# Performance work log

Measured on AMD Instinct MI355X. Metric: run time of the kernel, lower is better.

Reference implementation:

```python
import jax, jax.numpy as jnp
import numpy as np

EPS = 1e-6
NH, DK, DV = 4, 32, 32

def _ln2d(x, w, b):
    # LayerNorm2d: normalize over channel dim (dim=1), biased variance
    mu = jnp.mean(x, axis=1, keepdims=True)
    var = jnp.mean((x - mu) ** 2, axis=1, keepdims=True)
    y = (x - mu) / jnp.sqrt(var + EPS)
    return w[None, :, None, None] * y + b[None, :, None, None]

def _c1x1(w, x):
    # 1x1 conv == per-pixel matmul: w [out,in], x [B,C,H,W]
    return jnp.einsum('oc,bchw->bohw', w, x)

def _shifts(x, r):
    # All (2r+1)^2 zero-padded spatial shifts, row-major (dy,dx) like nn.Unfold.
    B, C, H, W = x.shape
    xp = jnp.pad(x, ((0, 0), (0, 0), (r, r), (r, r)))
    return jnp.stack([xp[:, :, dy:dy + H, dx:dx + W]
                      for dy in range(2 * r + 1) for dx in range(2 * r + 1)], axis=0)

def _local_attn(q, k, v, kernel):
    # Correlation-pyramid local attention: per-pixel q.k over kxk window of k,
    # softmax over window (temperature sqrt(d_k)), weighted sum of v window
    # (weights shared across channels, per ChannelAttention).
    B, _, H, W = q.shape
    r = (kernel - 1) // 2
    K2 = kernel * kernel
    qh = q.reshape(B, NH, DK, H, W)
    ks = _shifts(k, r).reshape(K2, B, NH, DK, H, W)
    corr = jnp.einsum('bncyx,jbncyx->jbnyx', qh, ks)            # [K2,B,NH,H,W]
    attn = jax.nn.softmax(corr / jnp.sqrt(jnp.float32(DK)), axis=0)
    vs = _shifts(v, r).reshape(K2, B, NH, DV, H, W)
    out = jnp.einsum('jbnyx,jbncyx->bncyx', attn, vs)
    return out.reshape(B, NH * DV, H, W)

def _mha(q, k, v, kernel, wq, wk, wv, fc, lnw, lnb):
    resid = q
    heads = _local_attn(_c1x1(wq, q), _c1x1(wk, k), _c1x1(wv, v), kernel)
    out = _c1x1(fc, heads) + resid   # residual BEFORE LN (per source)
    return _ln2d(out, lnw, lnb)

def _ffn(x, w1, b1, w2, b2, lnw, lnb):
    h = jax.nn.relu(_c1x1(w1, x) + b1[None, :, None, None])
    y = _c1x1(w2, h) + b2[None, :, None, None]
    return _ln2d(y, lnw, lnb) + x    # LN BEFORE residual add (per source)

def setup_inputs():
    key = jax.random.key(0)
    ks = jax.random.split(key, 24)
    B, C, H, W = 4, 128, 96, 96
    s = (2.0 / C) ** 0.5
    f = jnp.float32
    return {
        'input1': jax.random.normal(ks[0], (B, C, H, W), f),
        'input2': jax.random.normal(ks[1], (B, C, H, W), f),
        'wq_s': jax.random.normal(ks[2], (NH * DK, C), f) * s,
        'wk_s': jax.random.normal(ks[3], (NH * DK, C), f) * s,
        'wv_s': jax.random.normal(ks[4], (NH * DV, C), f) * s,
        'fc_s': jax.random.normal(ks[5], (C, NH * DV), f) * s,
        'lnw_s': jnp.ones((C,), f),
        'lnb_s': jnp.zeros((C,), f),
        'wq_c': jax.random.normal(ks[6], (NH * DK, C), f) * s,
        'wk_c': jax.random.normal(ks[7], (NH * DK, C), f) * s,
        'wv_c': jax.random.normal(ks[8], (NH * DV, C), f) * s,
        'fc_c': jax.random.normal(ks[9], (C, NH * DV), f) * s,
        'lnw_c': jnp.ones((C,), f),
        'lnb_c': jnp.zeros((C,), f),
        'w1': jax.random.normal(ks[10], (C, C), f) * s,
        'b1': jnp.zeros((C,), f),
        'w2': jax.random.normal(ks[11], (C, C), f) * s,
        'b2': jnp.zeros((C,), f),
        'lnw_f': jnp.ones((C,), f),
        'lnb_f': jnp.zeros((C,), f),
        'kernel': 5,
        'pad': 2,
    }

def reference(input1, input2, wq_s, wk_s, wv_s, fc_s, lnw_s, lnb_s,
              wq_c, wk_c, wv_c, fc_c, lnw_c, lnb_c,
              w1, b1, w2, b2, lnw_f, lnb_f, kernel, pad):
    slf1 = _mha(input1, input1, input1, kernel, wq_s, wk_s, wv_s, fc_s, lnw_s, lnb_s)
    slf2 = _mha(input2, input2, input2, kernel, wq_s, wk_s, wv_s, fc_s, lnw_s, lnb_s)
    crs1 = _mha(slf1, slf2, slf2, kernel, wq_c, wk_c, wv_c, fc_c, lnw_c, lnb_c)
    crs2 = _mha(slf2, slf1, slf1, kernel, wq_c, wk_c, wv_c, fc_c, lnw_c, lnb_c)
    out1 = _ffn(crs1, w1, b1, w2, b2, lnw_f, lnb_f)
    out2 = _ffn(crs2, w1, b1, w2, b2, lnw_f, lnb_f)
    return (out1, out2)
```

## Files before the change

kernel.cpp:

```cpp
#include <hip/hip_runtime.h>
#include <hip/hip_bf16.h>

typedef _Float16 h16;
typedef __attribute__((ext_vector_type(8))) _Float16 f16x8v;
typedef __attribute__((ext_vector_type(2))) _Float16 h2v;
typedef __attribute__((ext_vector_type(4))) float f32x4;
#define DI __device__ __forceinline__

constexpr int CH = 128;
constexpr int HH = 96, WW = 96;
constexpr int HW = HH * WW;
constexpr int NB = 4;
constexpr int NPIX = NB * HW;
constexpr int LDT = 136;
constexpr size_t HP = (size_t)NPIX * 32;
constexpr int GH = NPIX / 64;
constexpr int TY = 4, TX = 32;
constexpr int HYH = TY + 4, HXH = TX + 4;
constexpr int LDC = 40;
constexpr int ATB = NPIX / (TY * TX) * 4;

struct __attribute__((aligned(16))) h16x8 { h16 h[8]; };
struct Set { h16 *q, *k, *v; };

DI float h2f(h16 x) { return (float)x; }
DI h16   f2h(float x) { return (h16)x; }


DI void stage_x_cl(const h16* __restrict__ src, int ldx, h16* xl, int t) {
    #pragma unroll
    for (int i = 0; i < 4; ++i) {
        int id = t + 256 * i, px = id >> 4, cc = (id & 15) * 8;
        *reinterpret_cast<f16x8v*>(&xl[px * LDT + cc]) =
            *reinterpret_cast<const f16x8v*>(&src[(size_t)px * ldx + cc]);
    }
}

DI void stage_x_pl(const float* __restrict__ src, h16* xl, int t) {
    #pragma unroll
    for (int i = 0; i < 8; ++i) {
        int id = t + 256 * i, c = id >> 4, p4 = (id & 15) * 4;
        float4 v = *reinterpret_cast<const float4*>(&src[(size_t)c * HW + p4]);
        xl[(p4 + 0) * LDT + c] = f2h(v.x);
        xl[(p4 + 1) * LDT + c] = f2h(v.y);
        xl[(p4 + 2) * LDT + c] = f2h(v.z);
        xl[(p4 + 3) * LDT + c] = f2h(v.w);
    }
}

DI void stage_x_hm(const h16* __restrict__ Tq, h16* xl, int p0, int t) {
    const int px = t >> 2, c8 = (t & 3) * 8;
    #pragma unroll
    for (int h = 0; h < 4; ++h)
        *reinterpret_cast<f16x8v*>(&xl[px * LDT + h * 32 + c8]) =
            *reinterpret_cast<const f16x8v*>(&Tq[(size_t)h * HP + (size_t)(p0 + px) * 32 + c8]);
}

DI void stage_w(const float* __restrict__ w, h16* wl, int t) {
    #pragma unroll
    for (int i = 0; i < 8; ++i) {
        int id = t + 256 * i, o = id >> 4, cc = (id & 15) * 8;
        float4 a = *reinterpret_cast<const float4*>(&w[o * CH + cc]);
        float4 b = *reinterpret_cast<const float4*>(&w[o * CH + cc + 4]);
        h16x8 tmp;
        tmp.h[0] = f2h(a.x); tmp.h[1] = f2h(a.y); tmp.h[2] = f2h(a.z); tmp.h[3] = f2h(a.w);
        tmp.h[4] = f2h(b.x); tmp.h[5] = f2h(b.y); tmp.h[6] = f2h(b.z); tmp.h[7] = f2h(b.w);
        *reinterpret_cast<f16x8v*>(&wl[o * LDT + cc]) = *reinterpret_cast<const f16x8v*>(&tmp);
    }
}

DI void gemm64(const h16* xl, const h16* wl, int w, int l, f32x4* acc) {
    const int s = l & 15, g = l >> 4;
    #pragma unroll
    for (int ks = 0; ks < 4; ++ks) {
        f16x8v a = *reinterpret_cast<const f16x8v*>(&xl[(16 * w + s) * LDT + ks * 32 + g * 8]);
        #pragma unroll
        for (int n = 0; n < 8; ++n) {
            f16x8v b = *reinterpret_cast<const f16x8v*>(&wl[(16 * n + s) * LDT + ks * 32 + g * 8]);
            acc[n] = __builtin_amdgcn_mfma_f32_16x16x32_f16(a, b, acc[n], 0, 0, 0);
        }
    }
}

DI void qkv_epi(const f32x4* acc, h16* comp, int p0, int w, int l) {
    const int s = l & 15, g = l >> 4;
    #pragma unroll
    for (int n = 0; n < 8; ++n) {
        const int o = 16 * n + s, head = o >> 5, ch = o & 31;
        h16* pl = comp + (size_t)head * HP;
        #pragma unroll
        for (int j = 0; j < 4; ++j) {
            int px = 16 * w + 4 * g + j;
            pl[(size_t)(p0 + px) * 32 + ch] = f2h(acc[n][j]);
        }
    }
}

DI void ln128(float r[8][4], const float* gm, const float* bt, float val[8][4]) {
    #pragma unroll
    for (int j = 0; j < 4; ++j) {
        float sm = 0.f, sq = 0.f;
        #pragma unroll
        for (int n = 0; n < 8; ++n) { float v = r[n][j]; sm += v; sq += v * v; }
        sm += __shfl_xor(sm, 1); sq += __shfl_xor(sq, 1);
        sm += __shfl_xor(sm, 2); sq += __shfl_xor(sq, 2);
        sm += __shfl_xor(sm, 4); sq += __shfl_xor(sq, 4);
        sm += __shfl_xor(sm, 8); sq += __shfl_xor(sq, 8);
        const float mu = sm * (1.f / 128.f);
        const float var = sq * (1.f / 128.f) - mu * mu;
        const float rs = rsqrtf(var + 1e-6f);
        #pragma unroll
        for (int n = 0; n < 8; ++n)
            val[n][j] = gm[n] * (r[n][j] - mu) * rs + bt[n];
    }
}

__global__ __launch_bounds__(256, 2)
void qkv_self_b(const float* __restrict__ x0, const float* __restrict__ x1,
                const float* __restrict__ w0, const float* __restrict__ w1_,
                const float* __restrict__ w2_, Set sA, Set sB) {
    __shared__ h16 xl[64 * LDT];
    __shared__ h16 wl[CH * LDT];
    const int bid = blockIdx.x, half = bid / GH, p0 = (bid % GH) * 64;
    const float* xv = half ? x1 : x0;
    Set S = half ? sB : sA;
    const int t = threadIdx.x;
    const int b = p0 / HW, hw0 = p0 % HW;
    stage_x_pl(xv + (size_t)b * CH * HW + hw0, xl, t);
    const int w = t >> 6, l = t & 63;
    #pragma unroll
    for (int m = 0; m < 3; ++m) {
        const float* wm = (m == 0) ? w0 : ((m == 1) ? w1_ : w2_);
        h16* comp = (m == 0) ? S.q : ((m == 1) ? S.k : S.v);
        __syncthreads();
        stage_w(wm, wl, t);
        __syncthreads();
        f32x4 acc[8];
        #pragma unroll
        for (int n = 0; n < 8; ++n) acc[n] = {0.f, 0.f, 0.f, 0.f};
        gemm64(xl, wl, w, l, acc);
        qkv_epi(acc, comp, p0, w, l);
    }
}

__global__ __launch_bounds__(256)
void attn5b(Set s0, Set s1) {
    __shared__ h16 kv[HYH * HXH * LDC];
    const int bid = blockIdx.x, setId = bid / ATB, id = bid - setId * ATB;
    Set S = setId ? s1 : s0;
    const int n = id & 3, tile = id >> 2;
    const int img = tile / 72, rem = tile % 72, tr = rem / 3, tc = rem % 3;
    const int y0 = tr * TY, x0 = tc * TX;
    const int t = threadIdx.x;
    const int p = t >> 1, half = t & 1, ch16 = half * 16;
    const int ty = p >> 5, tx = p & 31;
    h16* Qh = S.q + (size_t)n * HP;
    const h16* Kh = S.k + (size_t)n * HP;
    const h16* Vh = S.v + (size_t)n * HP;
    const int gp = img * HW + (y0 + ty) * WW + (x0 + tx);
    h16* qp = Qh + (size_t)gp * 32 + ch16;

    f16x8v q0 = *reinterpret_cast<const f16x8v*>(qp);
    f16x8v q1 = *reinterpret_cast<const f16x8v*>(qp + 8);
    {
        const h16 sc = (h16)0.17677669529663689f;
        #pragma unroll
        for (int e = 0; e < 8; ++e) { q0[e] *= sc; q1[e] *= sc; }
    }

    #pragma unroll
    for (int i = 0; i < 5; ++i) {
        int id2 = t + 256 * i;
        if (id2 < 1152) {
            int r = id2 / 144, c = id2 - r * 144, px = c >> 2, c8 = (c & 3) * 8;
            int y = y0 + r - 2, x = x0 + px - 2;
            f16x8v v = {0, 0, 0, 0, 0, 0, 0, 0};
            if ((unsigned)y < (unsigned)HH && (unsigned)x < (unsigned)WW)
                v = *reinterpret_cast<const f16x8v*>(&Kh[((size_t)(img * HW + y * WW + x)) * 32 + c8]);
            *reinterpret_cast<f16x8v*>(&kv[(r * HXH + px) * LDC + c8]) = v;
        }
    }
    __syncthreads();

    float corr[25];
    #pragma unroll
    for (int dy = 0; dy < 5; ++dy)
        #pragma unroll
        for (int dx = 0; dx < 5; ++dx) {
            const h16* kp = &kv[((ty + dy) * HXH + tx + dx) * LDC + ch16];
            f16x8v k0 = *reinterpret_cast<const f16x8v*>(kp);
            f16x8v k1 = *reinterpret_cast<const f16x8v*>(kp + 8);
            float s;
#if __has_builtin(__builtin_amdgcn_fdot2)
            s = __builtin_amdgcn_fdot2(h2v{q0[0], q0[1]}, h2v{k0[0], k0[1]}, 0.f, false);
            s = __builtin_amdgcn_fdot2(h2v{q0[2], q0[3]}, h2v{k0[2], k0[3]}, s, false);
            s = __builtin_amdgcn_fdot2(h2v{q0[4], q0[5]}, h2v{k0[4], k0[5]}, s, false);
            s = __builtin_amdgcn_fdot2(h2v{q0[6], q0[7]}, h2v{k0[6], k0[7]}, s, false);
            s = __builtin_amdgcn_fdot2(h2v{q1[0], q1[1]}, h2v{k1[0], k1[1]}, s, false);
            s = __builtin_amdgcn_fdot2(h2v{q1[2], q1[3]}, h2v{k1[2], k1[3]}, s, false);
            s = __builtin_amdgcn_fdot2(h2v{q1[4], q1[5]}, h2v{k1[4], k1[5]}, s, false);
            s = __builtin_amdgcn_fdot2(h2v{q1[6], q1[7]}, h2v{k1[6], k1[7]}, s, false);
#else
            s = 0.f;
            #pragma unroll
            for (int e = 0; e < 8; ++e) s += h2f(q0[e]) * h2f(k0[e]);
            #pragma unroll
            for (int e = 0; e < 8; ++e) s += h2f(q1[e]) * h2f(k1[e]);
#endif
            s += __shfl_xor(s, 1);
            corr[dy * 5 + dx] = s;
        }

    float m = corr[0];
    #pragma unroll
    for (int j = 1; j < 25; ++j) m = fmaxf(m, corr[j]);
    float sum = 0.f;
    #pragma unroll
    for (int j = 0; j < 25; ++j) {
        float e = __expf(corr[j] - m);
        corr[j] = e; sum += e;
    }
    const float inv = 1.f / sum;

    __syncthreads();
    #pragma unroll
    for (int i = 0; i < 5; ++i) {
        int id2 = t + 256 * i;
        if (id2 < 1152) {
            int r = id2 / 144, c = id2 - r * 144, px = c >> 2, c8 = (c & 3) * 8;
            int y = y0 + r - 2, x = x0 + px - 2;
            f16x8v v = {0, 0, 0, 0, 0, 0, 0, 0};
            if ((unsigned)y < (unsigned)HH && (unsigned)x < (unsigned)WW)
                v = *reinterpret_cast<const f16x8v*>(&Vh[((size_t)(img * HW + y * WW + x)) * 32 + c8]);
            *reinterpret_cast<f16x8v*>(&kv[(r * HXH + px) * LDC + c8]) = v;
        }
    }
    __syncthreads();

    f16x8v o0 = {0, 0, 0, 0, 0, 0, 0, 0};
    f16x8v o1 = {0, 0, 0, 0, 0, 0, 0, 0};
    #pragma unroll
    for (int dy = 0; dy < 5; ++dy)
        #pragma unroll
        for (int dx = 0; dx < 5; ++dx) {
            const h16 ah = f2h(corr[dy * 5 + dx]);
            const f16x8v av = {ah, ah, ah, ah, ah, ah, ah, ah};
            const h16* vp = &kv[((ty + dy) * HXH + tx + dx) * LDC + ch16];
            f16x8v v0 = *reinterpret_cast<const f16x8v*>(vp);
            f16x8v v1 = *reinterpret_cast<const f16x8v*>(vp + 8);
            o0 += av * v0;
            o1 += av * v1;
        }
    {
        const h16 ih = f2h(inv);
        const f16x8v iv = {ih, ih, ih, ih, ih, ih, ih, ih};
        o0 *= iv; o1 *= iv;
    }
    *reinterpret_cast<f16x8v*>(qp)     = o0;
    *reinterpret_cast<f16x8v*>(qp + 8) = o1;
}

__global__ __launch_bounds__(256, 2)
void fcx_b(const h16* __restrict__ tA, const h16* __restrict__ tB,
           const float* __restrict__ in1, const float* __restrict__ in2,
           const float* __restrict__ wfc, const float* __restrict__ gamma,
           const float* __restrict__ beta,
           const float* __restrict__ wq, const float* __restrict__ wk,
           const float* __restrict__ wv,
           h16* __restrict__ x1g, h16* __restrict__ x2g, Set c1, Set c2) {
    __shared__ h16 xA[64 * LDT];
    __shared__ h16 xB[64 * LDT];
    __shared__ h16 wl[CH * LDT];
    const int t = threadIdx.x, p0 = blockIdx.x * 64;
    const int w = t >> 6, l = t & 63, s = l & 15, g4 = l >> 4;
    const int b = p0 / HW, hw0 = p0 % HW;

    stage_x_hm(tA, xA, p0, t);
    stage_x_hm(tB, xB, p0, t);
    stage_w(wfc, wl, t);
    __syncthreads();

    float gm[8], bt[8];
    #pragma unroll
    for (int n = 0; n < 8; ++n) { gm[n] = gamma[16 * n + s]; bt[n] = beta[16 * n + s]; }

    h16 vA[8][4], vB[8][4];
    {
        f32x4 acc[8];
        #pragma unroll
        for (int n = 0; n < 8; ++n) acc[n] = {0.f, 0.f, 0.f, 0.f};
        gemm64(xA, wl, w, l, acc);
        float r[8][4], val[8][4];
        #pragma unroll
        for (int n = 0; n < 8; ++n) {
            const int o = 16 * n + s;
            #pragma unroll
            for (int j = 0; j < 4; ++j) {
                const int px = 16 * w + 4 * g4 + j;
                r[n][j] = acc[n][j] +
                    in1[(size_t)b * CH * HW + (size_t)o * HW + hw0 + px];
            }
        }
        ln128(r, gm, bt, val);
        #pragma unroll
        for (int n = 0; n < 8; ++n)
            #pragma unroll
            for (int j = 0; j < 4; ++j) vA[n][j] = f2h(val[n][j]);
    }
    {
        f32x4 acc[8];
        #pragma unroll
        for (int n = 0; n < 8; ++n) acc[n] = {0.f, 0.f, 0.f, 0.f};
        gemm64(xB, wl, w, l, acc);
        float r[8][4], val[8][4];
        #pragma unroll
        for (int n = 0; n < 8; ++n) {
            const int o = 16 * n + s;
            #pragma unroll
            for (int j = 0; j < 4; ++j) {
                const int px = 16 * w + 4 * g4 + j;
                r[n][j] = acc[n][j] +
                    in2[(size_t)b * CH * HW + (size_t)o * HW + hw0 + px];
            }
        }
        ln128(r, gm, bt, val);
        #pragma unroll
        for (int n = 0; n < 8; ++n)
            #pragma unroll
            for (int j = 0; j < 4; ++j) vB[n][j] = f2h(val[n][j]);
    }
    __syncthreads();
    #pragma unroll
    for (int n = 0; n < 8; ++n) {
        const int o = 16 * n + s;
        #pragma unroll
        for (int j = 0; j < 4; ++j) {
            const int px = 16 * w + 4 * g4 + j;
            xA[px * LDT + o] = vA[n][j];
            xB[px * LDT + o] = vB[n][j];
            x1g[(size_t)(p0 + px) * CH + o] = vA[n][j];
            x2g[(size_t)(p0 + px) * CH + o] = vB[n][j];
        }
    }
    __syncthreads();

    stage_w(wq, wl, t);
    __syncthreads();
    {
        f32x4 acc[8];
        #pragma unroll
        for (int n = 0; n < 8; ++n) acc[n] = {0.f, 0.f, 0.f, 0.f};
        gemm64(xA, wl, w, l, acc);
        qkv_epi(acc, c1.q, p0, w, l);
    }
    {
        f32x4 acc[8];
        #pragma unroll
        for (int n = 0; n < 8; ++n) acc[n] = {0.f, 0.f, 0.f, 0.f};
        gemm64(xB, wl, w, l, acc);
        qkv_epi(acc, c2.q, p0, w, l);
    }
    __syncthreads();
    stage_w(wk, wl, t);
    __syncthreads();
    {
        f32x4 acc[8];
        #pragma unroll
        for (int n = 0; n < 8; ++n) acc[n] = {0.f, 0.f, 0.f, 0.f};
        gemm64(xB, wl, w, l, acc);
        qkv_epi(acc, c1.k, p0, w, l);
    }
    {
        f32x4 acc[8];
        #pragma unroll
        for (int n = 0; n < 8; ++n) acc[n] = {0.f, 0.f, 0.f, 0.f};
        gemm64(xA, wl, w, l, acc);
        qkv_epi(acc, c2.k, p0, w, l);
    }
    __syncthreads();
    stage_w(wv, wl, t);
    __syncthreads();
    {
        f32x4 acc[8];
        #pragma unroll
        for (int n = 0; n < 8; ++n) acc[n] = {0.f, 0.f, 0.f, 0.f};
        gemm64(xB, wl, w, l, acc);
        qkv_epi(acc, c1.v, p0, w, l);
    }
    {
        f32x4 acc[8];
        #pragma unroll
        for (int n = 0; n < 8; ++n) acc[n] = {0.f, 0.f, 0.f, 0.f};
        gemm64(xA, wl, w, l, acc);
        qkv_epi(acc, c2.v, p0, w, l);
    }
}

__global__ __launch_bounds__(256, 2)
void ffn_ln_b(const h16* __restrict__ t0, const h16* __restrict__ t1,
              const h16* __restrict__ x0, const h16* __restrict__ x1,
              const float* __restrict__ wfc, const float* __restrict__ gc,
              const float* __restrict__ bc,
              const float* __restrict__ w1m, const float* __restrict__ b1v,
              const float* __restrict__ w2m, const float* __restrict__ b2v,
              const float* __restrict__ gf, const float* __restrict__ bf,
              float* __restrict__ o0, float* __restrict__ o1) {
    __shared__ __align__(16) char smem[64 * LDT * 2 * 2 + CH * LDT * 2];
    h16*   xl = (h16*)smem;
    h16*   yl = (h16*)(smem + 64 * LDT * 2);
    h16*   wl = (h16*)(smem + 64 * LDT * 2 * 2);
    float* ll = (float*)(smem + 64 * LDT * 2 * 2);
    const int bid = blockIdx.x, half = bid / GH, p0 = (bid % GH) * 64;
    const h16* tin = half ? t1 : t0;
    const h16* xg  = half ? x1 : x0;
    float* outp = half ? o1 : o0;
    const int t = threadIdx.x;
    const int w = t >> 6, l = t & 63, s = l & 15, g4 = l >> 4;

    stage_x_hm(tin, xl, p0, t);
    stage_w(wfc, wl, t);
    __syncthreads();

    h16 yv[8][4];
    {
        f32x4 acc[8];
        #pragma unroll
        for (int n = 0; n < 8; ++n) acc[n] = {0.f, 0.f, 0.f, 0.f};
        gemm64(xl, wl, w, l, acc);
        float gm[8], bt[8], r[8][4], val[8][4];
        #pragma unroll
        for (int n = 0; n < 8; ++n) { gm[n] = gc[16 * n + s]; bt[n] = bc[16 * n + s]; }
        #pragma unroll
        for (int n = 0; n < 8; ++n) {
            const int o = 16 * n + s;
            #pragma unroll
            for (int j = 0; j < 4; ++j) {
                const int px = 16 * w + 4 * g4 + j;
                r[n][j] = acc[n][j] + h2f(xg[(size_t)(p0 + px) * CH + o]);
            }
        }
        ln128(r, gm, bt, val);
        #pragma unroll
        for (int n = 0; n < 8; ++n)
            #pragma unroll
            for (int j = 0; j < 4; ++j) yv[n][j] = f2h(val[n][j]);
    }
    __syncthreads();
    #pragma unroll
    for (int n = 0; n < 8; ++n) {
        const int o = 16 * n + s;
        #pragma unroll
        for (int j = 0; j < 4; ++j)
            yl[(16 * w + 4 * g4 + j) * LDT + o] = yv[n][j];
    }
    stage_w(w1m, wl, t);
    __syncthreads();

    {
        f32x4 acc[8];
        #pragma unroll
        for (int n = 0; n < 8; ++n) acc[n] = {0.f, 0.f, 0.f, 0.f};
        gemm64(yl, wl, w, l, acc);
        #pragma unroll
        for (int n = 0; n < 8; ++n) {
            const int o = 16 * n + s;
            const float bv = b1v[o];
            #pragma unroll
            for (int j = 0; j < 4; ++j)
                xl[(16 * w + 4 * g4 + j) * LDT + o] = f2h(fmaxf(acc[n][j] + bv, 0.f));
        }
    }
    __syncthreads();
    stage_w(w2m, wl, t);
    __syncthreads();

    float val[8][4];
    {
        f32x4 acc[8];
        #pragma unroll
        for (int n = 0; n < 8; ++n) acc[n] = {0.f, 0.f, 0.f, 0.f};
        gemm64(xl, wl, w, l, acc);
        float gm[8], bt[8], r[8][4];
        #pragma unroll
        for (int n = 0; n < 8; ++n) { gm[n] = gf[16 * n + s]; bt[n] = bf[16 * n + s]; }
        #pragma unroll
        for (int n = 0; n < 8; ++n) {
            const int o = 16 * n + s;
            const float bv = b2v[o];
            #pragma unroll
            for (int j = 0; j < 4; ++j) r[n][j] = acc[n][j] + bv;
        }
        ln128(r, gm, bt, val);
        #pragma unroll
        for (int n = 0; n < 8; ++n) {
            const int o = 16 * n + s;
            #pragma unroll
            for (int j = 0; j < 4; ++j)
                val[n][j] += h2f(yl[(16 * w + 4 * g4 + j) * LDT + o]);
        }
    }
    __syncthreads();
    #pragma unroll
    for (int n = 0; n < 8; ++n) {
        const int o = 16 * n + s;
        #pragma unroll
        for (int j = 0; j < 4; ++j) ll[o * 65 + 16 * w + 4 * g4 + j] = val[n][j];
    }
    __syncthreads();
    const int b = p0 / HW, hw0 = p0 % HW;
    #pragma unroll
    for (int i = 0; i < 8; ++i) {
        int id = t + 256 * i, c = id >> 4, p4 = (id & 15) * 4;
        float4 v = { ll[c * 65 + p4], ll[c * 65 + p4 + 1],
                     ll[c * 65 + p4 + 2], ll[c * 65 + p4 + 3] };
        *reinterpret_cast<float4*>(&outp[(size_t)b * CH * HW + (size_t)c * HW + hw0 + p4]) = v;
    }
}

extern "C" void kernel_launch(void* const* d_in, const int* in_sizes, int n_in,
                              void* d_out, int out_size, void* d_ws, size_t ws_size,
                              hipStream_t stream) {
    (void)in_sizes; (void)n_in; (void)out_size; (void)ws_size;
    const float* in1  = (const float*)d_in[0];
    const float* in2  = (const float*)d_in[1];
    const float* wq_s = (const float*)d_in[2];
    const float* wk_s = (const float*)d_in[3];
    const float* wv_s = (const float*)d_in[4];
    const float* fc_s = (const float*)d_in[5];
    const float* lnw_s= (const float*)d_in[6];
    const float* lnb_s= (const float*)d_in[7];
    const float* wq_c = (const float*)d_in[8];
    const float* wk_c = (const float*)d_in[9];
    const float* wv_c = (const float*)d_in[10];
    const float* fc_c = (const float*)d_in[11];
    const float* lnw_c= (const float*)d_in[12];
    const float* lnb_c= (const float*)d_in[13];
    const float* w1   = (const float*)d_in[14];
    const float* b1   = (const float*)d_in[15];
    const float* w2   = (const float*)d_in[16];
    const float* b2   = (const float*)d_in[17];
    const float* lnw_f= (const float*)d_in[18];
    const float* lnb_f= (const float*)d_in[19];

    const size_t BUF  = (size_t)NPIX * CH;
    const size_t BUFB = BUF * 2;
    char* ws = (char*)d_ws;
    h16* W0 = (h16*)(ws + 0 * BUFB);
    h16* W1 = (h16*)(ws + 1 * BUFB);
    h16* W2 = (h16*)(ws + 2 * BUFB);
    h16* W3 = (h16*)(ws + 3 * BUFB);
    h16* D0 = (h16*)d_out;
    h16* D1 = (h16*)((char*)d_out + 1 * BUFB);
    h16* D2 = (h16*)((char*)d_out + 2 * BUFB);
    h16* D3 = (h16*)((char*)d_out + 3 * BUFB);
    float* out1 = (float*)d_out;
    float* out2 = (float*)d_out + BUF;

    const dim3 B(256);

    Set SA = {W0, D0, D1};
    Set SB = {W1, D2, D3};
    h16* X1 = W2;
    h16* X2 = W3;
    Set C1 = {W0, D0, D1};
    Set C2 = {W1, D2, D3};

    qkv_self_b<<<dim3(2 * GH), B, 0, stream>>>(in1, in2, wq_s, wk_s, wv_s, SA, SB);
    attn5b<<<dim3(2 * ATB), B, 0, stream>>>(SA, SB);
    fcx_b<<<dim3(GH), B, 0, stream>>>(SA.q, SB.q, in1, in2,
                                      fc_s, lnw_s, lnb_s,
                                      wq_c, wk_c, wv_c, X1, X2, C1, C2);
    attn5b<<<dim3(2 * ATB), B, 0, stream>>>(C1, C2);
    ffn_ln_b<<<dim3(2 * GH), B, 0, stream>>>(C1.q, C2.q, X1, X2,
                                             fc_c, lnw_c, lnb_c,
                                             w1, b1, w2, b2, lnw_f, lnb_f,
                                             out1, out2);
}
```

Measured before the change: 156.9 us.

## Split fused FC/QKV kernel so each block handles one stream

Each block of the FC+LayerNorm+cross-QKV kernel now processes only one of the two input streams, chosen by block index, and the grid is doubled. This halves the per-block shared-memory footprint (one activation tile instead of two) and doubles the block count, to improve occupancy and load balance across CUs. The cost is that every block now stages the fc, wq, wk and wv weight tiles for half as much GEMM work. One redundant barrier before the first weight restage is also dropped.

```diff
diff --git a/kernel.cpp b/kernel.cpp
--- a/kernel.cpp
+++ b/kernel.cpp
@@ -261,36 +261,38 @@
 }
 
 __global__ __launch_bounds__(256, 2)
-void fcx_b(const h16* __restrict__ tA, const h16* __restrict__ tB,
-           const float* __restrict__ in1, const float* __restrict__ in2,
-           const float* __restrict__ wfc, const float* __restrict__ gamma,
-           const float* __restrict__ beta,
-           const float* __restrict__ wq, const float* __restrict__ wk,
-           const float* __restrict__ wv,
-           h16* __restrict__ x1g, h16* __restrict__ x2g, Set c1, Set c2) {
-    __shared__ h16 xA[64 * LDT];
-    __shared__ h16 xB[64 * LDT];
+void fcx1_b(const h16* __restrict__ tA, const h16* __restrict__ tB,
+            const float* __restrict__ in1, const float* __restrict__ in2,
+            const float* __restrict__ wfc, const float* __restrict__ gamma,
+            const float* __restrict__ beta,
+            const float* __restrict__ wq, const float* __restrict__ wk,
+            const float* __restrict__ wv,
+            h16* __restrict__ x1g, h16* __restrict__ x2g, Set c1, Set c2) {
+    __shared__ h16 xl[64 * LDT];
     __shared__ h16 wl[CH * LDT];
-    const int t = threadIdx.x, p0 = blockIdx.x * 64;
+    const int bid = blockIdx.x, half = bid / GH, p0 = (bid % GH) * 64;
+    const h16*   tin = half ? tB : tA;
+    const float* inr = half ? in2 : in1;
+    h16*         xg  = half ? x2g : x1g;
+    Set own   = half ? c2 : c1;
+    Set other = half ? c1 : c2;
+    const int t = threadIdx.x;
     const int w = t >> 6, l = t & 63, s = l & 15, g4 = l >> 4;
     const int b = p0 / HW, hw0 = p0 % HW;
 
-    stage_x_hm(tA, xA, p0, t);
-    stage_x_hm(tB, xB, p0, t);
+    stage_x_hm(tin, xl, p0, t);
     stage_w(wfc, wl, t);
     __syncthreads();
 
-    float gm[8], bt[8];
-    #pragma unroll
-    for (int n = 0; n < 8; ++n) { gm[n] = gamma[16 * n + s]; bt[n] = beta[16 * n + s]; }
-
-    h16 vA[8][4], vB[8][4];
-    {
-        f32x4 acc[8];
-        #pragma unroll
-        for (int n = 0; n < 8; ++n) acc[n] = {0.f, 0.f, 0.f, 0.f};
-        gemm64(xA, wl, w, l, acc);
-        float r[8][4], val[8][4];
+    h16 vX[8][4];
+    {
+        f32x4 acc[8];
+        #pragma unroll
+        for (int n = 0; n < 8; ++n) acc[n] = {0.f, 0.f, 0.f, 0.f};
+        gemm64(xl, wl, w, l, acc);
+        float gm[8], bt[8], r[8][4], val[8][4];
+        #pragma unroll
+        for (int n = 0; n < 8; ++n) { gm[n] = gamma[16 * n + s]; bt[n] = beta[16 * n + s]; }
         #pragma unroll
         for (int n = 0; n < 8; ++n) {
             const int o = 16 * n + s;
@@ -298,36 +300,14 @@
             for (int j = 0; j < 4; ++j) {
                 const int px = 16 * w + 4 * g4 + j;
                 r[n][j] = acc[n][j] +
-                    in1[(size_t)b * CH * HW + (size_t)o * HW + hw0 + px];
+                    inr[(size_t)b * CH * HW + (size_t)o * HW + hw0 + px];
             }
         }
         ln128(r, gm, bt, val);
         #pragma unroll
         for (int n = 0; n < 8; ++n)
             #pragma unroll
-            for (int j = 0; j < 4; ++j) vA[n][j] = f2h(val[n][j]);
-    }
-    {
-        f32x4 acc[8];
-        #pragma unroll
-        for (int n = 0; n < 8; ++n) acc[n] = {0.f, 0.f, 0.f, 0.f};
-        gemm64(xB, wl, w, l, acc);
-        float r[8][4], val[8][4];
-        #pragma unroll
-        for (int n = 0; n < 8; ++n) {
-            const int o = 16 * n + s;
-            #pragma unroll
-            for (int j = 0; j < 4; ++j) {
-                const int px = 16 * w + 4 * g4 + j;
-                r[n][j] = acc[n][j] +
-                    in2[(size_t)b * CH * HW + (size_t)o * HW + hw0 + px];
-            }
-        }
-        ln128(r, gm, bt, val);
-        #pragma unroll
-        for (int n = 0; n < 8; ++n)
-            #pragma unroll
-            for (int j = 0; j < 4; ++j) vB[n][j] = f2h(val[n][j]);
+            for (int j = 0; j < 4; ++j) vX[n][j] = f2h(val[n][j]);
     }
     __syncthreads();
     #pragma unroll
@@ -336,29 +316,18 @@
         #pragma unroll
         for (int j = 0; j < 4; ++j) {
             const int px = 16 * w + 4 * g4 + j;
-            xA[px * LDT + o] = vA[n][j];
-            xB[px * LDT + o] = vB[n][j];
-            x1g[(size_t)(p0 + px) * CH + o] = vA[n][j];
-            x2g[(size_t)(p0 + px) * CH + o] = vB[n][j];
-        }
-    }
-    __syncthreads();
-
+            xl[px * LDT + o] = vX[n][j];
+            xg[(size_t)(p0 + px) * CH + o] = vX[n][j];
+        }
+    }
     stage_w(wq, wl, t);
     __syncthreads();
     {
         f32x4 acc[8];
         #pragma unroll
         for (int n = 0; n < 8; ++n) acc[n] = {0.f, 0.f, 0.f, 0.f};
-        gemm64(xA, wl, w, l, acc);
-        qkv_epi(acc, c1.q, p0, w, l);
-    }
-    {
-        f32x4 acc[8];
-        #pragma unroll
-        for (int n = 0; n < 8; ++n) acc[n] = {0.f, 0.f, 0.f, 0.f};
-        gemm64(xB, wl, w, l, acc);
-        qkv_epi(acc, c2.q, p0, w, l);
+        gemm64(xl, wl, w, l, acc);
+        qkv_epi(acc, own.q, p0, w, l);
     }
     __syncthreads();
     stage_w(wk, wl, t);
@@ -367,15 +336,8 @@
         f32x4 acc[8];
         #pragma unroll
         for (int n = 0; n < 8; ++n) acc[n] = {0.f, 0.f, 0.f, 0.f};
-        gemm64(xB, wl, w, l, acc);
-        qkv_epi(acc, c1.k, p0, w, l);
-    }
-    {
-        f32x4 acc[8];
-        #pragma unroll
-        for (int n = 0; n < 8; ++n) acc[n] = {0.f, 0.f, 0.f, 0.f};
-        gemm64(xA, wl, w, l, acc);
-        qkv_epi(acc, c2.k, p0, w, l);
+        gemm64(xl, wl, w, l, acc);
+        qkv_epi(acc, other.k, p0, w, l);
     }
     __syncthreads();
     stage_w(wv, wl, t);
@@ -384,15 +346,8 @@
         f32x4 acc[8];
         #pragma unroll
         for (int n = 0; n < 8; ++n) acc[n] = {0.f, 0.f, 0.f, 0.f};
-        gemm64(xB, wl, w, l, acc);
-        qkv_epi(acc, c1.v, p0, w, l);
-    }
-    {
-        f32x4 acc[8];
-        #pragma unroll
-        for (int n = 0; n < 8; ++n) acc[n] = {0.f, 0.f, 0.f, 0.f};
-        gemm64(xA, wl, w, l, acc);
-        qkv_epi(acc, c2.v, p0, w, l);
+        gemm64(xl, wl, w, l, acc);
+        qkv_epi(acc, other.v, p0, w, l);
     }
 }
 
@@ -567,9 +522,9 @@
 
     qkv_self_b<<<dim3(2 * GH), B, 0, stream>>>(in1, in2, wq_s, wk_s, wv_s, SA, SB);
     attn5b<<<dim3(2 * ATB), B, 0, stream>>>(SA, SB);
-    fcx_b<<<dim3(GH), B, 0, stream>>>(SA.q, SB.q, in1, in2,
-                                      fc_s, lnw_s, lnb_s,
-                                      wq_c, wk_c, wv_c, X1, X2, C1, C2);
+    fcx1_b<<<dim3(2 * GH), B, 0, stream>>>(SA.q, SB.q, in1, in2,
+                                           fc_s, lnw_s, lnb_s,
+                                           wq_c, wk_c, wv_c, X1, X2, C1, C2);
     attn5b<<<dim3(2 * ATB), B, 0, stream>>>(C1, C2);
     ffn_ln_b<<<dim3(2 * GH), B, 0, stream>>>(C1.q, C2.q, X1, X2,
                                              fc_c, lnw_c, lnb_c,
```

Measured after the change: 153.9 us. No clear change (-1.9%).
